# Optimization experiments

Hardware: AMD Instinct MI355X
Metric: run time of the kernel (lower is better)

## Reference

```python
import jax, jax.numpy as jnp
import numpy as np

B = 4
N_SAMPLES = 32768
N_EVENTS = 32
N_HARMONICS = 16
SAMPLES_PER_FRAME = 256
N_FRAMES = N_SAMPLES // SAMPLES_PER_FRAME  # 128
SAMPLERATE = 22050
NYQ = SAMPLERATE // 2
MIN_F = 20.0 / NYQ
MAX_F = 4000.0 / NYQ
RES_BASE = 0.8
N_ROOMS = 8
LOG_SQRT_2PI = 0.5 * np.log(2.0 * np.pi).astype(np.float32)


def max_norm(x):
    return x / (jnp.max(jnp.abs(x), axis=-1, keepdims=True) + 1e-8)


def window(means, stds, n, mn, mx, eps=1e-8):
    # means/stds: [B, E, 1]; Normal pdf evaluated on linspace(0,1,n), max-normalized
    mu = mn + means * (mx - mn)
    sigma = eps + stds
    rng = jnp.linspace(0.0, 1.0, n, dtype=jnp.float32)[None, None, :]
    logp = -0.5 * ((rng - mu) / sigma) ** 2 - jnp.log(sigma) - LOG_SQRT_2PI
    return max_norm(jnp.exp(logp))


def interp_linear(x, out_size):
    # F.interpolate(mode='linear', align_corners=False) along last axis
    in_size = x.shape[-1]
    coords = (jnp.arange(out_size, dtype=jnp.float32) + 0.5) * (in_size / out_size) - 0.5
    coords = jnp.clip(coords, 0.0, in_size - 1.0)
    lo = jnp.floor(coords).astype(jnp.int32)
    hi = jnp.minimum(lo + 1, in_size - 1)
    w = (coords - lo.astype(jnp.float32))
    return x[..., lo] * (1.0 - w) + x[..., hi] * w


def fft_convolve(a, b):
    # zero-padded linear convolution via FFT, truncated to original length
    n = a.shape[-1]
    pa = jnp.pad(a, [(0, 0)] * (a.ndim - 1) + [(0, n)])
    pb = jnp.pad(b, [(0, 0)] * (b.ndim - 1) + [(0, n)])
    out = jnp.fft.irfft(jnp.fft.rfft(pa) * jnp.fft.rfft(pb), n=2 * n)
    return out[..., :n]


def setup_inputs():
    key = jax.random.key(0)
    k1, k2, k3, k4, k5 = jax.random.split(key, 5)
    return {
        'event_params': jax.random.uniform(k1, (B, N_EVENTS, N_HARMONICS + 6), dtype=jnp.float32),
        'mx_raw': jax.random.normal(k2, (B,), dtype=jnp.float32),
        'room_logits': jax.random.normal(k3, (B, N_ROOMS), dtype=jnp.float32),
        'noise': jax.random.uniform(k4, (1, 1, N_SAMPLES), dtype=jnp.float32, minval=-1.0, maxval=1.0),
        'impulse_responses': jax.random.normal(k5, (N_ROOMS, N_SAMPLES), dtype=jnp.float32) * 0.01,
    }


def reference(event_params, mx_raw, room_logits, noise, impulse_responses):
    b = event_params.shape[0]
    ep = event_params  # [B, E, 22], already in [0,1] (post-activation)
    freq_means = ep[:, :, 0:1] ** 2
    freq_stds = ep[:, :, 1:2] * 0.1
    time_means = ep[:, :, 2:3]
    time_stds = ep[:, :, 3:4] * 0.1
    f0 = ep[:, :, 4:5] ** 2
    amps = ep[:, :, 5:6] ** 2
    res = ep[:, :, 6:] * (1.0 - RES_BASE) + RES_BASE  # [B, E, H]
    mx = jax.nn.sigmoid(mx_raw).reshape(b, 1, 1)
    rooms = jax.nn.softmax(room_logits, axis=-1)

    # --- BandLimitedNoise ---
    nfft = N_SAMPLES // 2 + 1
    win = window(freq_means, freq_stds, nfft, MIN_F, MAX_F)  # [B, E, nfft]
    noise_spec = jnp.fft.rfft(noise, norm='ortho')            # [1, 1, nfft]
    bl_noise = jnp.fft.irfft(noise_spec * win, n=N_SAMPLES, norm='ortho')  # [B, E, N]

    # --- impulse (time) windows ---
    events = window(time_means, time_stds, N_SAMPLES, 0.0, 1.0)  # [B, E, N]

    # --- Resonance ---
    factors = jnp.arange(1, N_HARMONICS + 1, dtype=jnp.float32)
    f0s = MIN_F + (MAX_F - MIN_F) * f0                 # [B, E, 1]
    freqs = f0s * factors                               # [B, E, H]
    freqs = jnp.where(freqs >= 1.0, 0.0, freqs)
    freqs_fr = jnp.broadcast_to(freqs[..., None], freqs.shape + (N_FRAMES,))
    freqs_s = interp_linear(freqs_fr, N_SAMPLES)        # [B, E, H, N]
    res_fr = jnp.cumprod(jnp.broadcast_to(res[..., None], res.shape + (N_FRAMES,)), axis=-1)
    res_s = interp_linear(res_fr, N_SAMPLES)            # [B, E, H, N]
    resonances = jnp.sum(res_s * jnp.sin(jnp.cumsum(freqs_s * (2.0 * np.pi), axis=-1)), axis=2)  # [B, E, N]

    # --- locate events + resonance convolution (noise_coeff = 1) ---
    located = bl_noise * events * amps
    located = fft_convolve(located, resonances) + located
    located = jnp.sum(located, axis=1, keepdims=True)   # [B, 1, N]

    # --- reverb: rooms-weighted impulse response, dry/wet mix ---
    dry = located
    imp = jnp.einsum('br,rn->bn', rooms, impulse_responses)[:, None, :]
    wet = fft_convolve(located, imp)
    return dry * (1.0 - mx) + wet * mx
```

## Files before the change

### kernel.cpp

```cpp
#include <hip/hip_runtime.h>
#include <math.h>

#define NSAMP 32768
#define NPAD  65536
#define NCH   128
#define TWO_PI 6.2831853071795864f
#define MINF ((float)(20.0/11025.0))
#define DRF  ((float)(4000.0/11025.0 - 20.0/11025.0))

__device__ __forceinline__ float2 cxmul(float2 a, float2 b){
    return make_float2(a.x*b.x - a.y*b.y, a.x*b.y + a.y*b.x);
}

template<int DIR>
__device__ __forceinline__ void fft4v(float2* v, int i0, int i1, int i2, int i3){
    float2 a=v[i0], b=v[i1], c=v[i2], d=v[i3];
    float2 t0 = make_float2(a.x+c.x, a.y+c.y);
    float2 t1 = make_float2(a.x-c.x, a.y-c.y);
    float2 t2 = make_float2(b.x+d.x, b.y+d.y);
    float2 t3 = make_float2(b.x-d.x, b.y-d.y);
    v[i0] = make_float2(t0.x+t2.x, t0.y+t2.y);
    v[i2] = make_float2(t0.x-t2.x, t0.y-t2.y);
    if (DIR < 0) {
        v[i1] = make_float2(t1.x + t3.y, t1.y - t3.x);
        v[i3] = make_float2(t1.x - t3.y, t1.y + t3.x);
    } else {
        v[i1] = make_float2(t1.x - t3.y, t1.y + t3.x);
        v[i3] = make_float2(t1.x + t3.y, t1.y - t3.x);
    }
}

template<int DIR>
__device__ __forceinline__ void twm(float2& v, float c, float s){
    float sy = (DIR<0) ? -s : s;
    v = cxmul(v, make_float2(c, sy));
}

template<int DIR>
__device__ __forceinline__ void fft16r(float2* v){
    const float C1=0.92387953251128674f, S1=0.38268343236508978f, H=0.70710678118654752f;
    fft4v<DIR>(v,0,4,8,12);
    fft4v<DIR>(v,1,5,9,13);
    fft4v<DIR>(v,2,6,10,14);
    fft4v<DIR>(v,3,7,11,15);
    twm<DIR>(v[5],  C1, S1);
    twm<DIR>(v[6],  H,  H);
    twm<DIR>(v[7],  S1, C1);
    twm<DIR>(v[9],  H,  H);
    twm<DIR>(v[10], 0.0f, 1.0f);
    twm<DIR>(v[11], -H, H);
    twm<DIR>(v[13], S1, C1);
    twm<DIR>(v[14], -H, H);
    twm<DIR>(v[15], -C1, -S1);
    fft4v<DIR>(v,0,1,2,3);
    fft4v<DIR>(v,4,5,6,7);
    fft4v<DIR>(v,8,9,10,11);
    fft4v<DIR>(v,12,13,14,15);
}

template<int DIR>
__device__ __forceinline__ void fft8r(float2* v){
    const float H=0.70710678118654752f;
    #pragma unroll
    for (int n1=0;n1<4;n1++){
        float2 t=v[n1], u=v[n1+4];
        v[n1]   = make_float2(t.x+u.x, t.y+u.y);
        v[n1+4] = make_float2(t.x-u.x, t.y-u.y);
    }
    twm<DIR>(v[5], H, H);
    twm<DIR>(v[6], 0.0f, 1.0f);
    twm<DIR>(v[7], -H, H);
    fft4v<DIR>(v,0,1,2,3);
    fft4v<DIR>(v,4,5,6,7);
}

__device__ __forceinline__ int slot16(int r){ return ((r&3)<<2)|(r>>2); }
__device__ __forceinline__ int slot8(int r){ return ((r&1)<<2)|(r>>1); }
__device__ __forceinline__ int lxs(int l){ return l ^ ((l>>4)&15); }

template<int R>
__device__ __forceinline__ void twiddle(float2* v, float ang1){
    float s,c; __sincosf(ang1,&s,&c);
    float2 w[R];
    w[1] = make_float2(c,s);
    #pragma unroll
    for (int r=2;r<R;r++) w[r] = cxmul(w[r>>1], w[r-(r>>1)]);
    #pragma unroll
    for (int r=1;r<R;r++) v[r] = cxmul(v[r], w[r]);
}

template<int DIR>
__device__ __forceinline__ void n1_tail(float2 (&v)[16], float2* lds, int t, int p,
                                        float2* __restrict__ out)
{
    fft16r<DIR>(v);
    #pragma unroll
    for (int r=0;r<16;r++) lds[lxs(256*(t>>4) + 16*(t&15) + r)] = v[slot16(r)];
    __syncthreads();
    #pragma unroll
    for (int q=0;q<16;q++) v[q] = lds[lxs(256*q + t)];
    int jm = t & 15;
    if (jm) twiddle<16>(v, (DIR<0?-TWO_PI:TWO_PI)*(float)jm*(1.0f/256.0f));
    fft16r<DIR>(v);
    int j2 = 256*p + t;
    float2* yo = out + (j2>>4)*256 + (j2&15);
    #pragma unroll
    for (int r=0;r<16;r++) yo[16*r] = v[slot16(r)];
}

__global__ __launch_bounds__(256) void mfk_n1_noise_setup(const float* __restrict__ noise,
        float2* __restrict__ dst, const float* __restrict__ EP,
        const float* __restrict__ MXR, const float* __restrict__ RL,
        float* __restrict__ chP, unsigned* __restrict__ chQ, float* __restrict__ chR,
        float* __restrict__ cum, float* __restrict__ mxA, float* __restrict__ rmA)
{
    __shared__ float2 lds[4096];
    int t = threadIdx.x, px = blockIdx.x;
    if (px >= 8){
        int q = (px-8)*256 + t;
        int c = q >> 4, h = q & 15;
        const float* P = EP + c*22;
        const float LSQ = (float)0.9189385332046727;
        float f0m = __fmul_rn(P[4],P[4]);
        float f0s = __fadd_rn(MINF, __fmul_rn(f0m, DRF));
        float fr  = __fmul_rn(f0s, (float)(h+1));
        if (fr >= 1.0f) fr = 0.0f;
        chQ[q] = (unsigned)(unsigned long long)((double)fr*4294967296.0 + 0.5);
        float rs = __fadd_rn(__fmul_rn(P[6+h],0.2f),0.8f);
        chR[q] = rs;
        float cp = rs;
        float* crow = cum + (size_t)q*128;
        for (int jj=0;jj<128;jj++){ crow[jj] = cp; cp = __fmul_rn(cp, rs); }
        if (h == 0){
            float fm  = __fmul_rn(P[0],P[0]);
            float fmu = __fadd_rn(MINF, __fmul_rn(fm, DRF));
            float fsg = 1e-8f + P[1]*0.1f;
            float fsi = 1.0f/fsg;
            int i0 = (int)floorf(fmu*16384.0f + 0.5f);
            i0 = min(max(i0,0),16384);
            float rg = (float)i0 * (1.0f/16384.0f);
            float tt = (rg - fmu)*fsi;
            float Lc = logf(fsg) + LSQ;
            float sc = expf(-Lc) / (expf(-0.5f*tt*tt - Lc) + 1e-8f);
            float tmu = P[2];
            float tsg = 1e-8f + P[3]*0.1f;
            float tsi = 1.0f/tsg;
            int i1 = (int)floorf(tmu*32767.0f + 0.5f);
            i1 = min(max(i1,0),32767);
            float rg1 = (float)((double)i1 * (1.0/32767.0));
            float tt1 = (rg1 - tmu)*tsi;
            float Lc1 = logf(tsg) + LSQ;
            float sc1 = expf(-Lc1) / (expf(-0.5f*tt1*tt1 - Lc1) + 1e-8f);
            float amp = P[5]*P[5];
            float* o = chP + c*8;
            o[0]=fmu; o[1]=fsi; o[2]=sc; o[3]=tmu; o[4]=tsi; o[5]=sc1; o[6]=amp; o[7]=0.f;
        }
        if (q < 4){
            int b = q;
            mxA[b] = 1.0f/(1.0f + expf(-MXR[b]));
            const float* rl = RL + b*8;
            float mx = rl[0];
            for (int r=1;r<8;r++) mx = fmaxf(mx, rl[r]);
            float sum=0.f;
            float e2[8];
            for (int r=0;r<8;r++){ e2[r]=expf(rl[r]-mx); sum+=e2[r]; }
            for (int r=0;r<8;r++) rmA[b*8+r] = e2[r]/sum;
        }
        return;
    }
    int p = px;
    int j = 128*(t>>4) + 16*p + (t&15);
    float2 v[16];
    #pragma unroll
    for (int r=0;r<16;r++) v[r] = make_float2(noise[j + 2048*r], 0.0f);
    n1_tail<-1>(v, lds, t, p, dst);
}

__global__ __launch_bounds__(256) void mfk_n1_specwin(const float2* __restrict__ nspec,
        const float* __restrict__ chP, float2* __restrict__ dst, int g0)
{
    __shared__ float2 lds[4096];
    int t = threadIdx.x, p = blockIdx.x, pr = blockIdx.y;
    int c0 = g0 + 2*pr;
    const float* A = chP + c0*8;
    const float* B = chP + (c0+1)*8;
    float a0=A[0], a1=A[1], a2=A[2], b0=B[0], b1=B[1], b2=B[2];
    int j = 128*(t>>4) + 16*p + (t&15);
    float2 v[16];
    #pragma unroll
    for (int r=0;r<16;r++){
        int k = j + 2048*r;
        int kw = (k <= 16384) ? k : (32768 - k);
        float rg = (float)kw * (1.0f/16384.0f);
        float t0 = (rg - a0)*a1;
        float w0 = expf(-0.5f*t0*t0)*a2;
        float t1 = (rg - b0)*b1;
        float w1 = expf(-0.5f*t1*t1)*b2;
        float2 N = nspec[k];
        v[r] = make_float2(N.x*w0 - N.y*w1, N.y*w0 + N.x*w1);
    }
    n1_tail<1>(v, lds, t, p, dst + (size_t)pr*NSAMP);
}

template<int DIR>
__device__ __forceinline__ void n2_stageC(const float2* __restrict__ x, float2* lds, int t, int p)
{
    float2 v[16];
    int j2 = 256*(t>>5) + 32*p + (t&31);
    #pragma unroll
    for (int r=0;r<16;r++) v[r] = x[j2 + 2048*r];
    int jm = 32*p + (t&31);
    if (jm) twiddle<16>(v, (DIR<0?-TWO_PI:TWO_PI)*(float)jm*(1.0f/4096.0f));
    fft16r<DIR>(v);
    #pragma unroll
    for (int r=0;r<16;r++) lds[lxs(256*r + t)] = v[slot16(r)];
    __syncthreads();
}

template<int DIR>
__device__ __forceinline__ int n2_stageD(float2* lds, int t, int p, int u, float2 (&w8)[8])
{
    int q = t + 256*u;
    int j3 = ((q>>5)<<8) + 32*p + (q&31);
    #pragma unroll
    for (int r3=0;r3<8;r3++) w8[r3] = lds[lxs(256*(q>>5) + 32*r3 + (q&31))];
    if (j3) twiddle<8>(w8, (DIR<0?-TWO_PI:TWO_PI)*(float)j3*(1.0f/32768.0f));
    fft8r<DIR>(w8);
    return j3;
}

__global__ __launch_bounds__(256) void mfk_n2_noise(const float2* __restrict__ src,
                                                    float2* __restrict__ dst)
{
    __shared__ float2 lds[4096];
    int t = threadIdx.x, p = blockIdx.x;
    n2_stageC<-1>(src, lds, t, p);
    #pragma unroll
    for (int u=0;u<2;u++){
        float2 w8[8];
        int j3 = n2_stageD<-1>(lds, t, p, u, w8);
        #pragma unroll
        for (int r=0;r<8;r++) dst[j3 + 4096*r] = w8[slot8(r)];
    }
}

__global__ __launch_bounds__(256) void mfk_n2_unpack(const float2* __restrict__ src,
        const float* __restrict__ chP, float* __restrict__ locraw, int g0)
{
    __shared__ float2 lds[4096];
    int t = threadIdx.x, p = blockIdx.x, pr = blockIdx.y;
    n2_stageC<1>(src + (size_t)pr*NSAMP, lds, t, p);
    int lc0 = 2*pr;
    const float* C0 = chP + (g0+lc0)*8;
    const float* C1 = chP + (g0+lc0+1)*8;
    float c03=C0[3], c04=C0[4], c05=C0[5], c06=C0[6];
    float c13=C1[3], c14=C1[4], c15=C1[5], c16=C1[6];
    #pragma unroll
    for (int u=0;u<2;u++){
        float2 w8[8];
        int j3 = n2_stageD<1>(lds, t, p, u, w8);
        #pragma unroll
        for (int r=0;r<8;r++){
            int n = j3 + 4096*r;
            float2 val = w8[slot8(r)];
            float rg = (float)((double)n * (1.0/32767.0));
            float tt0 = (rg - c03)*c04;
            float ew0 = expf(-0.5f*tt0*tt0)*c05;
            float tt1 = (rg - c13)*c14;
            float ew1 = expf(-0.5f*tt1*tt1)*c15;
            locraw[(size_t)lc0*NSAMP + n]     = val.x*(1.0f/32768.0f)*ew0*c06;
            locraw[(size_t)(lc0+1)*NSAMP + n] = val.y*(1.0f/32768.0f)*ew1*c16;
        }
    }
}

__global__ __launch_bounds__(256) void mfk_packZres_f01(const float* __restrict__ locraw,
        const unsigned* __restrict__ chQ, const float* __restrict__ chR,
        const float* __restrict__ cum, float2* __restrict__ dst, int g0)
{
    __shared__ float2 lds[4096];
    float* cumS = (float*)lds;
    __shared__ unsigned qS[16];
    __shared__ float rS[16];
    int t = threadIdx.x, p = blockIdx.x, lc = blockIdx.y;
    int cg = g0 + lc;
    const float* crow = cum + (size_t)cg*2048;
    #pragma unroll
    for (int i=0;i<8;i++) cumS[t + 256*i] = crow[t + 256*i];
    if (t < 16){ qS[t] = chQ[cg*16 + t]; rS[t] = chR[cg*16 + t]; }
    __syncthreads();
    int j = 256*(t>>4) + 16*p + (t&15);
    float co0 = ((float)j + 0.5f)*0.00390625f - 0.5f;
    float fl = floorf(co0);
    float wf = co0 - fl;
    int ilo = (int)fl;
    float acc[8];
    #pragma unroll
    for (int r=0;r<8;r++) acc[r] = 0.0f;
    if (j == 0) acc[0] = 1.0f;
    unsigned T1 = (unsigned)(j+1);
    #pragma unroll
    for (int hh=0; hh<16; hh++){
        unsigned qq = qS[hh];
        float rs = rS[hh];
        float rs2 = rs*rs, rs4 = rs2*rs2, rs8 = rs4*rs4, rs16 = rs8*rs8;
        float mix = fmaf(rs - 1.0f, wf, 1.0f);
        const float* cr = cumS + hh*128;
        unsigned bits = qq * T1;
        unsigned step = qq << 12;
        float e_cur = (ilo >= 0) ? cr[ilo] : cr[15];
        float env0  = (ilo >= 0) ? 0.0f    : cr[0];
        #pragma unroll
        for (int r=0;r<8;r++){
            float env;
            if (r == 0 && ilo < 0) env = env0;
            else env = (ilo == 15 && r == 7) ? e_cur : e_cur*mix;
            float m = (float)bits * 2.3283064365386963e-10f;
            float sv; asm("v_sin_f32 %0, %1" : "=v"(sv) : "v"(m));
            acc[r] = fmaf(env, sv, acc[r]);
            bits += step;
            if (!(r == 0 && ilo < 0)) e_cur *= rs16;
        }
    }
    const float* la = locraw + (size_t)lc*NSAMP;
    float2 v[16];
    #pragma unroll
    for (int r=0;r<8;r++) v[r] = make_float2(la[j + 4096*r], acc[r]);
    #pragma unroll
    for (int r=8;r<16;r++) v[r] = make_float2(0.f,0.f);
    __syncthreads();
    n1_tail<-1>(v, lds, t, p, dst + (size_t)lc*NPAD);
}

template<int DIR, int NSTORE>
__global__ __launch_bounds__(256) void mfk_f23(const float2* __restrict__ src,
                                               float2* __restrict__ dst)
{
    __shared__ float2 lds[4096];
    int t = threadIdx.x, p = blockIdx.x;
    size_t boff = (size_t)blockIdx.y * NPAD;
    int a = t>>4, w = t&15;
    int j = 256*a + 16*p + w;
    const float2* x = src + boff;
    float2 v[16];
    #pragma unroll
    for (int r=0;r<16;r++) v[r] = x[j + 4096*r];
    int jm = 16*p + w;
    if (jm) twiddle<16>(v, (DIR<0?-TWO_PI:TWO_PI)*(float)jm*(1.0f/4096.0f));
    fft16r<DIR>(v);
    #pragma unroll
    for (int r=0;r<16;r++) lds[lxs(256*a + 16*r + w)] = v[slot16(r)];
    __syncthreads();
    #pragma unroll
    for (int q=0;q<16;q++) v[q] = lds[lxs(256*q + t)];
    if (j) twiddle<16>(v, (DIR<0?-TWO_PI:TWO_PI)*(float)j*(1.0f/65536.0f));
    fft16r<DIR>(v);
    float2* yo = dst + boff + j;
    #pragma unroll
    for (int r=0;r<NSTORE;r++) yo[4096*r] = v[slot16(r)];
}

__global__ __launch_bounds__(256) void mfk_prodacc(const float2* __restrict__ Z,
        float2* __restrict__ T, int g0, int G, int addTo)
{
    int x = blockIdx.x;
    int beta = blockIdx.y;
    int z = blockIdx.z;
    int g = ((x>>4)<<3) | (x&7);
    int kb = (x&8) ? (255 - g) : g;
    int k = kb*256 + threadIdx.x;
    int km = (NPAD - k) & (NPAD-1);
    int cstart = max(64*beta + 32*z, g0);
    int cend   = min(64*beta + 32*z + 32, g0+G);
    float2 S0 = make_float2(0.f,0.f), S1 = make_float2(0.f,0.f);
    #pragma unroll 4
    for (int c=cstart; c<cend; ++c){
        const float2* zp = Z + (size_t)(c-g0)*NPAD;
        float2 a = zp[k], am = zp[km];
        float2 A0 = make_float2(0.5f*(a.x+am.x), 0.5f*(a.y-am.y));
        float2 R0 = make_float2(0.5f*(a.y+am.y), -0.5f*(a.x-am.x));
        float2 P = cxmul(A0,R0);
        if ((c>>5)&1){ S1.x += P.x; S1.y += P.y; }
        else         { S0.x += P.x; S0.y += P.y; }
    }
    const float s = 1.0f/65536.0f;
    float2 q = make_float2((S0.x - S1.y)*s, (S0.y + S1.x)*s);
    size_t idx = ((size_t)z*2 + beta)*NPAD + k;
    if (addTo){ float2 o = T[idx]; q.x += o.x; q.y += o.y; }
    T[idx] = q;
}

__global__ __launch_bounds__(256) void mfk_plain_f01(const float2* __restrict__ T,
        float2* __restrict__ dst)
{
    __shared__ float2 lds[4096];
    int t = threadIdx.x, p = blockIdx.x, b = blockIdx.y;
    const float2* x0 = T + (size_t)b*NPAD;
    const float2* x1 = T + (size_t)(2+b)*NPAD;
    int j = 256*(t>>4) + 16*p + (t&15);
    float2 v[16];
    #pragma unroll
    for (int r=0;r<16;r++){
        float2 u0 = x0[j + 4096*r], u1 = x1[j + 4096*r];
        v[r] = make_float2(u0.x+u1.x, u0.y+u1.y);
    }
    n1_tail<1>(v, lds, t, p, dst + (size_t)b*NPAD);
}

__global__ __launch_bounds__(256) void mfk_dry_f01(const float2* __restrict__ U2,
        const float* __restrict__ rmA, const float* __restrict__ IR, float2* __restrict__ dst)
{
    __shared__ float2 lds[4096];
    int t = threadIdx.x, p = blockIdx.x, b = blockIdx.y;
    int j = 256*(t>>4) + 16*p + (t&15);
    float rm[8];
    #pragma unroll
    for (int r=0;r<8;r++) rm[r] = rmA[b*8+r];
    const float2* Ub = U2 + (size_t)(b>>1)*NPAD;
    float2 v[16];
    #pragma unroll
    for (int r=0;r<8;r++){
        int n = j + 4096*r;
        float2 lcv = Ub[n];
        float locv = (b&1) ? lcv.y : lcv.x;
        float iv = 0.f;
        #pragma unroll
        for (int q=0;q<8;q++) iv += rm[q]*IR[(size_t)q*NSAMP + n];
        v[r] = make_float2(locv, iv);
    }
    #pragma unroll
    for (int r=8;r<16;r++) v[r] = make_float2(0.f,0.f);
    n1_tail<-1>(v, lds, t, p, dst + (size_t)b*NPAD);
}

__global__ __launch_bounds__(256) void mfk_prod_f01(const float2* __restrict__ Z,
        float2* __restrict__ dst)
{
    __shared__ float2 lds[4096];
    int t = threadIdx.x;
    int px = blockIdx.x;
    int p = (px < 8) ? px : 23 - px;
    int pr = blockIdx.y;
    const float2* z0 = Z + (size_t)(2*pr)*NPAD;
    const float2* z1 = z0 + NPAD;
    int j = 256*(t>>4) + 16*p + (t&15);
    float2 v[16];
    #pragma unroll
    for (int r=0;r<16;r++){
        int k = j + 4096*r;
        int km = (NPAD - k) & (NPAD-1);
        float2 a = z0[k], am = z0[km];
        float2 A0 = make_float2(0.5f*(a.x+am.x), 0.5f*(a.y-am.y));
        float2 R0 = make_float2(0.5f*(a.y+am.y), -0.5f*(a.x-am.x));
        float2 P0 = cxmul(A0,R0);
        float2 b = z1[k], bm = z1[km];
        float2 A1 = make_float2(0.5f*(b.x+bm.x), 0.5f*(b.y-bm.y));
        float2 R1 = make_float2(0.5f*(b.y+bm.y), -0.5f*(b.x-bm.x));
        float2 P1 = cxmul(A1,R1);
        const float s = 1.0f/65536.0f;
        v[r] = make_float2((P0.x - P1.y)*s, (P0.y + P1.x)*s);
    }
    n1_tail<1>(v, lds, t, p, dst + (size_t)pr*NPAD);
}

__global__ __launch_bounds__(256) void mfk_f23_final(const float2* __restrict__ src,
        const float2* __restrict__ U2, const float* __restrict__ mxA,
        float* __restrict__ out)
{
    __shared__ float2 lds[4096];
    int t = threadIdx.x, p = blockIdx.x;
    int pr = blockIdx.y;
    size_t boff = (size_t)pr * NPAD;
    int a = t>>4, w = t&15;
    int j = 256*a + 16*p + w;
    const float2* x = src + boff;
    float2 v[16];
    #pragma unroll
    for (int r=0;r<16;r++) v[r] = x[j + 4096*r];
    int jm = 16*p + w;
    if (jm) twiddle<16>(v, TWO_PI*(float)jm*(1.0f/4096.0f));
    fft16r<1>(v);
    #pragma unroll
    for (int r=0;r<16;r++) lds[lxs(256*a + 16*r + w)] = v[slot16(r)];
    __syncthreads();
    #pragma unroll
    for (int q=0;q<16;q++) v[q] = lds[lxs(256*q + t)];
    if (j) twiddle<16>(v, TWO_PI*(float)j*(1.0f/65536.0f));
    fft16r<1>(v);
    int b0 = 2*pr, b1 = b0+1;
    float mx0 = mxA[b0], mx1 = mxA[b1];
    const float2* Ub = U2 + (size_t)pr*NPAD;
    #pragma unroll
    for (int r=0;r<8;r++){
        int ts = j + 4096*r;
        float2 val = v[slot16(r)];
        float2 dry = Ub[ts];
        out[(size_t)b0*NSAMP+ts] = dry.x*(1.f-mx0) + val.x*mx0;
        out[(size_t)b1*NSAMP+ts] = dry.y*(1.f-mx1) + val.y*mx1;
    }
}

extern "C" void kernel_launch(void* const* d_in, const int* in_sizes, int n_in,
                              void* d_out, int out_size, void* d_ws, size_t ws_size,
                              hipStream_t stream)
{
    (void)in_sizes; (void)n_in; (void)out_size;
    const float* EP   = (const float*)d_in[0];
    const float* MXR  = (const float*)d_in[1];
    const float* RL   = (const float*)d_in[2];
    const float* NOISE= (const float*)d_in[3];
    const float* IR   = (const float*)d_in[4];
    float* out = (float*)d_out;
    char* w = (char*)d_ws;

    auto need = [](long long g)->long long {
        return 2LL*g*NPAD*8 + 1LL*g*NSAMP*4 + (long long)NSAMP*8
             + 2048LL*128*4 + (128LL*8 + 2048 + 2048 + 4 + 32)*4
             + 4LL*NPAD*8  + 2LL*NPAD*8  + 16384;
    };
    int G = 128;
    while (G > 4 && need(G) > (long long)ws_size) G >>= 1;

    size_t off = 0;
    auto alloc = [&](size_t bytes)->char* {
        char* p = w + off; off += (bytes + 255) & ~(size_t)255; return p;
    };
    float2*   arA    = (float2*)alloc((size_t)G*NPAD*8);
    float2*   arB    = (float2*)alloc((size_t)G*NPAD*8);
    float*    locraw = (float*) alloc((size_t)G*NSAMP*4);
    float2*   T      = (float2*)alloc(4LL*NPAD*8);
    float2*   U2     = (float2*)alloc(2LL*NPAD*8);
    float2*   nspec  = (float2*)alloc((size_t)NSAMP*8);
    float*    cum    = (float*) alloc(2048LL*128*4);
    float*    chP    = (float*) alloc(128*8*4);
    unsigned* chQ    = (unsigned*)alloc(2048*4);
    float*    chR    = (float*) alloc(2048*4);
    float*    mxA    = (float*) alloc(4*4);
    float*    rmA    = (float*) alloc(32*4);

    mfk_n1_noise_setup<<<dim3(16),256,0,stream>>>(NOISE, arB, EP, MXR, RL,
                                                  chP, chQ, chR, cum, mxA, rmA);
    mfk_n2_noise<<<dim3(8),256,0,stream>>>(arB, nspec);

    for (int g0 = 0; g0 < NCH; g0 += G){
        int P = G/2;
        mfk_n1_specwin<<<dim3(8,P),256,0,stream>>>(nspec, chP, arA, g0);
        mfk_n2_unpack<<<dim3(8,P),256,0,stream>>>(arA, chP, locraw, g0);
        mfk_packZres_f01<<<dim3(16,G),256,0,stream>>>(locraw, chQ, chR, cum, arA, g0);
        mfk_f23<-1,16><<<dim3(16,G),256,0,stream>>>(arA, arB);
        mfk_prodacc<<<dim3(256,2,2),256,0,stream>>>(arB, T, g0, G, (g0>0)?1:0);
    }

    mfk_plain_f01<<<dim3(16,2),256,0,stream>>>(T, arB);
    mfk_f23<1,8><<<dim3(16,2),256,0,stream>>>(arB, U2);

    mfk_dry_f01<<<dim3(16,4),256,0,stream>>>(U2, rmA, IR, arA);
    mfk_f23<-1,16><<<dim3(16,4),256,0,stream>>>(arA, arB);
    mfk_prod_f01<<<dim3(16,2),256,0,stream>>>(arB, arA);
    mfk_f23_final<<<dim3(16,2),256,0,stream>>>(arA, U2, mxA, out);
}
```

Baseline: 177.6 us.

## Transpose cum layout, fuse inverse FFT stage with dry packing, halve channel group

```diff
diff --git a/kernel.cpp b/kernel.cpp
--- a/kernel.cpp
+++ b/kernel.cpp
@@ -129,8 +129,7 @@
         float rs = __fadd_rn(__fmul_rn(P[6+h],0.2f),0.8f);
         chR[q] = rs;
         float cp = rs;
-        float* crow = cum + (size_t)q*128;
-        for (int jj=0;jj<128;jj++){ crow[jj] = cp; cp = __fmul_rn(cp, rs); }
+        for (int jj=0;jj<128;jj++){ cum[(size_t)jj*2048 + q] = cp; cp = __fmul_rn(cp, rs); }
         if (h == 0){
             float fm  = __fmul_rn(P[0],P[0]);
             float fmu = __fadd_rn(MINF, __fmul_rn(fm, DRF));
@@ -280,13 +279,15 @@
 {
     __shared__ float2 lds[4096];
     float* cumS = (float*)lds;
-    __shared__ unsigned qS[16];
-    __shared__ float rS[16];
+    unsigned* qS = (unsigned*)(cumS + 2048);
+    float* rS = cumS + 2064;
     int t = threadIdx.x, p = blockIdx.x, lc = blockIdx.y;
     int cg = g0 + lc;
-    const float* crow = cum + (size_t)cg*2048;
-    #pragma unroll
-    for (int i=0;i<8;i++) cumS[t + 256*i] = crow[t + 256*i];
+    #pragma unroll
+    for (int i=0;i<8;i++){
+        int jj = (t>>4) + 16*i;
+        cumS[jj*16 + (t&15)] = cum[(size_t)jj*2048 + cg*16 + (t&15)];
+    }
     if (t < 16){ qS[t] = chQ[cg*16 + t]; rS[t] = chR[cg*16 + t]; }
     __syncthreads();
     int j = 256*(t>>4) + 16*p + (t&15);
@@ -305,11 +306,10 @@
         float rs = rS[hh];
         float rs2 = rs*rs, rs4 = rs2*rs2, rs8 = rs4*rs4, rs16 = rs8*rs8;
         float mix = fmaf(rs - 1.0f, wf, 1.0f);
-        const float* cr = cumS + hh*128;
         unsigned bits = qq * T1;
         unsigned step = qq << 12;
-        float e_cur = (ilo >= 0) ? cr[ilo] : cr[15];
-        float env0  = (ilo >= 0) ? 0.0f    : cr[0];
+        float e_cur = (ilo >= 0) ? cumS[ilo*16 + hh] : cumS[15*16 + hh];
+        float env0  = (ilo >= 0) ? 0.0f : cumS[hh];
         #pragma unroll
         for (int r=0;r<8;r++){
             float env;
@@ -407,30 +407,57 @@
     n1_tail<1>(v, lds, t, p, dst + (size_t)b*NPAD);
 }
 
-__global__ __launch_bounds__(256) void mfk_dry_f01(const float2* __restrict__ U2,
-        const float* __restrict__ rmA, const float* __restrict__ IR, float2* __restrict__ dst)
-{
-    __shared__ float2 lds[4096];
-    int t = threadIdx.x, p = blockIdx.x, b = blockIdx.y;
-    int j = 256*(t>>4) + 16*p + (t&15);
-    float rm[8];
-    #pragma unroll
-    for (int r=0;r<8;r++) rm[r] = rmA[b*8+r];
-    const float2* Ub = U2 + (size_t)(b>>1)*NPAD;
-    float2 v[16];
+__global__ __launch_bounds__(256) void mfk_f23U2_dry(const float2* __restrict__ src,
+        const float* __restrict__ rmA, const float* __restrict__ IR,
+        float2* __restrict__ U2, float2* __restrict__ dstA)
+{
+    __shared__ float2 lds[4096];
+    int t = threadIdx.x, p = blockIdx.x, pr = blockIdx.y;
+    size_t boff = (size_t)pr * NPAD;
+    int a = t>>4, w = t&15;
+    int j = 256*a + 16*p + w;
+    const float2* x = src + boff;
+    float2 v[16];
+    #pragma unroll
+    for (int r=0;r<16;r++) v[r] = x[j + 4096*r];
+    int jm = 16*p + w;
+    if (jm) twiddle<16>(v, TWO_PI*(float)jm*(1.0f/4096.0f));
+    fft16r<1>(v);
+    #pragma unroll
+    for (int r=0;r<16;r++) lds[lxs(256*a + 16*r + w)] = v[slot16(r)];
+    __syncthreads();
+    #pragma unroll
+    for (int q=0;q<16;q++) v[q] = lds[lxs(256*q + t)];
+    if (j) twiddle<16>(v, TWO_PI*(float)j*(1.0f/65536.0f));
+    fft16r<1>(v);
+    float tvx[8], tvy[8];
     #pragma unroll
     for (int r=0;r<8;r++){
-        int n = j + 4096*r;
-        float2 lcv = Ub[n];
-        float locv = (b&1) ? lcv.y : lcv.x;
-        float iv = 0.f;
+        int ts = j + 4096*r;
+        float2 val = v[slot16(r)];
+        U2[boff + ts] = val;
+        tvx[r] = val.x; tvy[r] = val.y;
+    }
+    #pragma unroll
+    for (int s=0;s<2;s++){
+        int b = 2*pr + s;
+        float rm[8];
         #pragma unroll
-        for (int q=0;q<8;q++) iv += rm[q]*IR[(size_t)q*NSAMP + n];
-        v[r] = make_float2(locv, iv);
-    }
-    #pragma unroll
-    for (int r=8;r<16;r++) v[r] = make_float2(0.f,0.f);
-    n1_tail<-1>(v, lds, t, p, dst + (size_t)b*NPAD);
+        for (int r=0;r<8;r++) rm[r] = rmA[b*8+r];
+        float2 vv[16];
+        #pragma unroll
+        for (int r=0;r<8;r++){
+            int n = j + 4096*r;
+            float iv = 0.f;
+            #pragma unroll
+            for (int q=0;q<8;q++) iv += rm[q]*IR[(size_t)q*NSAMP + n];
+            vv[r] = make_float2(s ? tvy[r] : tvx[r], iv);
+        }
+        #pragma unroll
+        for (int r=8;r<16;r++) vv[r] = make_float2(0.f,0.f);
+        __syncthreads();
+        n1_tail<-1>(vv, lds, t, p, dstA + (size_t)b*NPAD);
+    }
 }
 
 __global__ __launch_bounds__(256) void mfk_prod_f01(const float2* __restrict__ Z,
@@ -518,7 +545,7 @@
              + 2048LL*128*4 + (128LL*8 + 2048 + 2048 + 4 + 32)*4
              + 4LL*NPAD*8  + 2LL*NPAD*8  + 16384;
     };
-    int G = 128;
+    int G = 64;
     while (G > 4 && need(G) > (long long)ws_size) G >>= 1;
 
     size_t off = 0;
@@ -552,9 +579,7 @@
     }
 
     mfk_plain_f01<<<dim3(16,2),256,0,stream>>>(T, arB);
-    mfk_f23<1,8><<<dim3(16,2),256,0,stream>>>(arB, U2);
-
-    mfk_dry_f01<<<dim3(16,4),256,0,stream>>>(U2, rmA, IR, arA);
+    mfk_f23U2_dry<<<dim3(16,2),256,0,stream>>>(arB, rmA, IR, U2, arA);
     mfk_f23<-1,16><<<dim3(16,4),256,0,stream>>>(arA, arB);
     mfk_prod_f01<<<dim3(16,2),256,0,stream>>>(arB, arA);
     mfk_f23_final<<<dim3(16,2),256,0,stream>>>(arA, U2, mxA, out);
```

Result: slower. 208.3 us (+17.3%).
